# Performance work log

Hardware: AMD Instinct MI355X
Metric: run time of the kernel (lower is better)

## Reference

```python
import jax, jax.numpy as jnp
import numpy as np

NEG = -1e30  # effective -inf in float32, safe under logaddexp grads
EPS = 1e-7   # keras.backend.epsilon()


def _ctc_loss(y_pred, y_true):
    """Faithful port of keras.backend.ctc_batch_cost with full-length
    input_length=T and label_length=L (as the CTCLayer sets them).
    y_pred: [B, T, C] post-softmax probabilities; blank = C-1.
    y_true: [B, L] int labels in [0, C-1).
    Returns loss [B, 1].
    """
    logp = jnp.log(y_pred + EPS)            # keras takes log(prob + eps)
    B, T, C = y_pred.shape
    L = y_true.shape[1]
    S = 2 * L + 1
    blank = C - 1

    # Extended label sequence: blank, l1, blank, l2, ..., blank  -> [B, S]
    ext = jnp.full((B, S), blank, dtype=y_true.dtype).at[:, 1::2].set(y_true)
    # Per-time emission log-probs of extended symbols: [B, T, S]
    lp_ext = jnp.take_along_axis(logp, ext[:, None, :], axis=2)

    # Skip transition s-2 -> s allowed when ext[s] != blank and ext[s] != ext[s-2]
    prev2_ext = jnp.pad(ext[:, :-2], ((0, 0), (2, 0)), constant_values=-1)
    allow_skip = (ext != blank) & (ext != prev2_ext)  # [B, S]

    # alpha init at t=0
    alpha = jnp.full((B, S), NEG, dtype=logp.dtype)
    alpha = alpha.at[:, 0].set(lp_ext[:, 0, 0]).at[:, 1].set(lp_ext[:, 0, 1])

    def step(alpha, lp_t):
        shift1 = jnp.pad(alpha[:, :-1], ((0, 0), (1, 0)), constant_values=NEG)
        shift2 = jnp.pad(alpha[:, :-2], ((0, 0), (2, 0)), constant_values=NEG)
        shift2 = jnp.where(allow_skip, shift2, NEG)
        new = jnp.logaddexp(jnp.logaddexp(alpha, shift1), shift2) + lp_t
        return new, None

    lp_seq = jnp.moveaxis(lp_ext[:, 1:, :], 1, 0)  # [T-1, B, S]
    alpha, _ = jax.lax.scan(step, alpha, lp_seq)

    # Terminate in final blank or final label
    loss = -jnp.logaddexp(alpha[:, S - 1], alpha[:, S - 2])  # [B]
    return loss[:, None]  # keras returns [B, 1]


def setup_inputs() -> dict:
    key = jax.random.key(0)
    k1, k2 = jax.random.split(key)
    B, T, C, L = 256, 256, 1000, 64
    y_true = jax.random.randint(k1, (B, L), 0, C - 1, dtype=jnp.int64)
    logits = jax.random.normal(k2, (B, T, C), dtype=jnp.float32)
    y_pred = jax.nn.softmax(logits, axis=-1)  # module expects softmax probs
    return {"y_true": y_true, "y_pred": y_pred}


def reference(y_true, y_pred):
    return _ctc_loss(y_pred, y_true)
```

## Files before the change

kernel.cpp:

```cpp
#include <hip/hip_runtime.h>


#define T_    256
#define C_    1000
#define L_    64
#define BLANK 999
#define NEGF  (-1e30f)
#define EPSF  (1e-7f)
#define PD    8

__global__ __launch_bounds__(64)
void ctc_fwd_kernel(const int* __restrict__ y_true,
                    const float* __restrict__ y_pred,
                    float* __restrict__ out) {
    const int b    = blockIdx.x;
    const int lane = threadIdx.x;

    const float* __restrict__ yp = y_pred + (size_t)b * T_ * C_;

    const int lab   = y_true[b * L_ + lane];
    const int labm1 = __shfl_up(lab, 1, 64);
    const bool allow = (lane > 0) && (lab != labm1);

    float aE, aO, aL;
    {
        float pb = yp[BLANK];
        float pl = yp[lab];
        aE = (lane == 0) ? __logf(pb + EPSF) : NEGF;
        aO = (lane == 0) ? __logf(pl + EPSF) : NEGF;
        aL = NEGF;
    }

    float pbB[PD], pbL[PD];
    #pragma unroll
    for (int k = 0; k < PD; ++k) {
        int t = 1 + k; if (t > T_ - 1) t = T_ - 1;
        const float* p = yp + t * C_;
        pbB[k] = p[BLANK];
        pbL[k] = p[lab];
    }

    for (int tb = 1; tb < T_; tb += PD) {
        #pragma unroll
        for (int j = 0; j < PD; ++j) {
            const int t = tb + j;
            if (t >= T_) break;

            int tn = t + PD; if (tn > T_ - 1) tn = T_ - 1;
            const float* pn = yp + tn * C_;
            float nB = pn[BLANK];
            float nL = pn[lab];

            const float lpB = __logf(pbB[j] + EPSF);
            const float lpL = __logf(pbL[j] + EPSF);

            float upO = __shfl_up(aO, 1, 64);
            if (lane == 0) upO = NEGF;

            float mE = fmaxf(aE, upO);
            float nE = mE + __logf(__expf(aE - mE) + __expf(upO - mE)) + lpB;

            float sk = allow ? upO : NEGF;
            float mO = fmaxf(fmaxf(aO, aE), sk);
            float nO = mO + __logf(__expf(aO - mO) + __expf(aE - mO) +
                                   __expf(sk - mO)) + lpL;

            float mL = fmaxf(aL, aO);
            float nL2 = mL + __logf(__expf(aL - mL) + __expf(aO - mL)) + lpB;

            aE = nE; aO = nO; aL = nL2;
            pbB[j] = nB; pbL[j] = nL;
        }
    }

    if (lane == 63) {
        float m = fmaxf(aL, aO);
        out[b] = -(m + __logf(__expf(aL - m) + __expf(aO - m)));
    }
}

extern "C" void kernel_launch(void* const* d_in, const int* in_sizes, int n_in,
                              void* d_out, int out_size, void* d_ws, size_t ws_size,
                              hipStream_t stream) {
    const int*   y_true = (const int*)d_in[0];
    const float* y_pred = (const float*)d_in[1];
    float*       out    = (float*)d_out;
    (void)in_sizes; (void)n_in; (void)d_ws; (void)ws_size; (void)out_size;

    ctc_fwd_kernel<<<dim3(256), dim3(64), 0, stream>>>(y_true, y_pred, out);
}
```

Before: 382.8 us.

## Split CTC into parallel gather/log kernel and compact-buffer scan kernel

Adds a highly parallel pre-pass that gathers the blank and label probabilities for every (batch, time) pair, takes their logs, and writes them into a compact 66-float-per-row workspace. The sequential scan kernel then reads this contiguous buffer instead of doing scattered gathers over the 1000-wide probability rows, and no longer computes logs on its critical path. The aim is to take the latency-bound scattered loads and log work off the serial 256-step recurrence, which ran on only 256 single-wave blocks. The cost is an extra kernel launch and a workspace write and read.

```diff
diff --git a/kernel.cpp b/kernel.cpp
--- a/kernel.cpp
+++ b/kernel.cpp
@@ -7,37 +7,53 @@
 #define BLANK 999
 #define NEGF  (-1e30f)
 #define EPSF  (1e-7f)
+#define RS    66
 #define PD    8
 
+__global__ __launch_bounds__(256)
+void ctc_gather_kernel(const int* __restrict__ y_true,
+                       const float* __restrict__ y_pred,
+                       float* __restrict__ lp) {
+    const int wave = threadIdx.x >> 6;
+    const int lane = threadIdx.x & 63;
+    const int pair = blockIdx.x * 4 + wave;
+    const int b = pair >> 8;
+    const int t = pair & 255;
+
+    const int lab = y_true[b * L_ + lane];
+    const float* __restrict__ row = y_pred + (size_t)pair * C_;
+    float* __restrict__ orow = lp + (size_t)pair * RS;
+
+    float v = row[lab];
+    orow[1 + lane] = __logf(v + EPSF);
+    if (lane == 0) {
+        orow[0] = __logf(row[BLANK] + EPSF);
+    }
+}
+
 __global__ __launch_bounds__(64)
-void ctc_fwd_kernel(const int* __restrict__ y_true,
-                    const float* __restrict__ y_pred,
-                    float* __restrict__ out) {
+void ctc_scan_kernel(const int* __restrict__ y_true,
+                     const float* __restrict__ lp,
+                     float* __restrict__ out) {
     const int b    = blockIdx.x;
     const int lane = threadIdx.x;
 
-    const float* __restrict__ yp = y_pred + (size_t)b * T_ * C_;
+    const float* __restrict__ lrow = lp + (size_t)b * T_ * RS;
 
     const int lab   = y_true[b * L_ + lane];
     const int labm1 = __shfl_up(lab, 1, 64);
     const bool allow = (lane > 0) && (lab != labm1);
 
-    float aE, aO, aL;
-    {
-        float pb = yp[BLANK];
-        float pl = yp[lab];
-        aE = (lane == 0) ? __logf(pb + EPSF) : NEGF;
-        aO = (lane == 0) ? __logf(pl + EPSF) : NEGF;
-        aL = NEGF;
-    }
+    float aE = (lane == 0) ? lrow[0] : NEGF;
+    float aO = (lane == 0) ? lrow[1] : NEGF;
+    float aL = NEGF;
 
-    float pbB[PD], pbL[PD];
+    float pB[PD], pL[PD];
     #pragma unroll
     for (int k = 0; k < PD; ++k) {
         int t = 1 + k; if (t > T_ - 1) t = T_ - 1;
-        const float* p = yp + t * C_;
-        pbB[k] = p[BLANK];
-        pbL[k] = p[lab];
+        pB[k] = lrow[t * RS];
+        pL[k] = lrow[t * RS + 1 + lane];
     }
 
     for (int tb = 1; tb < T_; tb += PD) {
@@ -47,12 +63,11 @@
             if (t >= T_) break;
 
             int tn = t + PD; if (tn > T_ - 1) tn = T_ - 1;
-            const float* pn = yp + tn * C_;
-            float nB = pn[BLANK];
-            float nL = pn[lab];
+            float nB = lrow[tn * RS];
+            float nL = lrow[tn * RS + 1 + lane];
 
-            const float lpB = __logf(pbB[j] + EPSF);
-            const float lpL = __logf(pbL[j] + EPSF);
+            const float lpB = pB[j];
+            const float lpL = pL[j];
 
             float upO = __shfl_up(aO, 1, 64);
             if (lane == 0) upO = NEGF;
@@ -69,7 +84,7 @@
             float nL2 = mL + __logf(__expf(aL - mL) + __expf(aO - mL)) + lpB;
 
             aE = nE; aO = nO; aL = nL2;
-            pbB[j] = nB; pbL[j] = nL;
+            pB[j] = nB; pL[j] = nL;
         }
     }
 
@@ -85,7 +100,9 @@
     const int*   y_true = (const int*)d_in[0];
     const float* y_pred = (const float*)d_in[1];
     float*       out    = (float*)d_out;
-    (void)in_sizes; (void)n_in; (void)d_ws; (void)ws_size; (void)out_size;
+    float*       lp     = (float*)d_ws;
+    (void)in_sizes; (void)n_in; (void)ws_size; (void)out_size;
 
-    ctc_fwd_kernel<<<dim3(256), dim3(64), 0, stream>>>(y_true, y_pred, out);
+    ctc_gather_kernel<<<dim3((256 * 256) / 4), dim3(256), 0, stream>>>(y_true, y_pred, lp);
+    ctc_scan_kernel<<<dim3(256), dim3(64), 0, stream>>>(y_true, lp, out);
 }
```

After: 405.8 us. +6.0%, slower.
